# Performance work log

Measured on AMD Instinct MI355X. Metric: run time of the kernel, lower is better.

## Reference

```python
import jax, jax.numpy as jnp
from jax import lax
import numpy as np

INPUT = 80
H1 = 100
H2 = 50


def _lstm_layer(x, Wih, Whh, bih, bhh):
    """PyTorch-semantics single-layer LSTM, batch_first.
    x: [B,T,I]; Wih: [4H,I]; Whh: [4H,H]; biases: [4H]. Gate order: i,f,g,o.
    Returns full hidden sequence [B,T,H]."""
    B, T, _ = x.shape
    H = Whh.shape[1]
    # precompute input projections for all timesteps (one big GEMM)
    pre = jnp.einsum('bti,gi->tbg', x, Wih) + (bih + bhh)  # [T,B,4H]

    def step(carry, p):
        h, c = carry
        gates = p + h @ Whh.T  # [B,4H]
        i, f, g, o = jnp.split(gates, 4, axis=-1)
        i = jax.nn.sigmoid(i)
        f = jax.nn.sigmoid(f)
        g = jnp.tanh(g)
        o = jax.nn.sigmoid(o)
        c = f * c + i * g
        h = o * jnp.tanh(c)
        return (h, c), h

    h0 = jnp.zeros((B, H), x.dtype)
    (_, _), hs = lax.scan(step, (h0, h0), pre)  # hs: [T,B,H]
    return jnp.transpose(hs, (1, 0, 2))  # [B,T,H]


def setup_inputs() -> dict:
    key = jax.random.key(0)
    ks = jax.random.split(key, 9)
    B, T = 1024, 512
    s1 = 1.0 / np.sqrt(H1)
    s2 = 1.0 / np.sqrt(H2)
    return {
        'x': jax.random.normal(ks[0], (B, T, INPUT), dtype=jnp.float32),
        'Wih1': jax.random.uniform(ks[1], (4 * H1, INPUT), jnp.float32, -s1, s1),
        'Whh1': jax.random.uniform(ks[2], (4 * H1, H1), jnp.float32, -s1, s1),
        'bih1': jax.random.uniform(ks[3], (4 * H1,), jnp.float32, -s1, s1),
        'bhh1': jax.random.uniform(ks[4], (4 * H1,), jnp.float32, -s1, s1),
        'Wih2': jax.random.uniform(ks[5], (4 * H2, H1), jnp.float32, -s2, s2),
        'Whh2': jax.random.uniform(ks[6], (4 * H2, H2), jnp.float32, -s2, s2),
        'bih2': jax.random.uniform(ks[7], (4 * H2,), jnp.float32, -s2, s2),
        'bhh2': jax.random.uniform(ks[8], (4 * H2,), jnp.float32, -s2, s2),
    }


def reference(x, Wih1, Whh1, bih1, bhh1, Wih2, Whh2, bih2, bhh2):
    # Dropout layers are identity in eval mode.
    h1 = _lstm_layer(x, Wih1, Whh1, bih1, bhh1)   # [B,T,100]
    h2 = _lstm_layer(h1, Wih2, Whh2, bih2, bhh2)  # [B,T,50]
    return h2[:, -1, :]                            # [B,50]
```

## Files before the change

kernel.cpp:

```cpp
#include <hip/hip_runtime.h>

#define BT 1024
#define TT 512

__device__ __forceinline__ float sig_(float x) { return 1.f / (1.f + __expf(-x)); }
__device__ __forceinline__ float th_(float x)  { return 1.f - 2.f / (1.f + __expf(2.f * x)); }

#define PIN4(v) asm volatile("" : "+v"((v).x), "+v"((v).y), "+v"((v).z), "+v"((v).w))
#define PIN2(v) asm volatile("" : "+v"((v).x), "+v"((v).y))

template <int KS, int KPAD, int KH, int N, bool XMODE>
__device__ __forceinline__ void gp_stage(
    const float* __restrict__ A, const float* __restrict__ W,
    float (&As)[128][KPAD], float (&Bs)[KPAD][64],
    int tid, int n0, int by, int t0, int k0)
{
    constexpr int NQH = KH / 4;
#pragma unroll
    for (int ii = tid; ii < 128 * NQH; ii += 256) {
        int r = ii / NQH, q = ii % NQH;
        const float* src;
        if (XMODE) {
            int b  = (by & 7) * 128 + r;
            int tl = by >> 3;
            src = A + ((size_t)b * TT + (t0 + tl)) * KS;
        } else {
            src = A + (size_t)(by * 128 + r) * KS;
        }
        float4 v = *(const float4*)(src + k0 + q * 4);
        As[r][q * 4 + 0] = v.x; As[r][q * 4 + 1] = v.y;
        As[r][q * 4 + 2] = v.z; As[r][q * 4 + 3] = v.w;
    }
#pragma unroll
    for (int ii = tid; ii < 64 * NQH; ii += 256) {
        int n = ii & 63, kq = ii >> 6;
        float4 v = make_float4(0.f, 0.f, 0.f, 0.f);
        if (n0 + n < N) v = *(const float4*)(W + (size_t)(n0 + n) * KS + k0 + kq * 4);
        Bs[kq * 4 + 0][n] = v.x; Bs[kq * 4 + 1][n] = v.y;
        Bs[kq * 4 + 2][n] = v.z; Bs[kq * 4 + 3][n] = v.w;
    }
}

template <int KPAD, int KH>
__device__ __forceinline__ void gp_compute(
    const float (&As)[128][KPAD], const float (&Bs)[KPAD][64],
    float (&acc)[8][4], int tx, int ty)
{
    for (int kk = 0; kk < KH; kk += 4) {
        float4 bv0 = *(const float4*)&Bs[kk + 0][tx * 4];
        float4 bv1 = *(const float4*)&Bs[kk + 1][tx * 4];
        float4 bv2 = *(const float4*)&Bs[kk + 2][tx * 4];
        float4 bv3 = *(const float4*)&Bs[kk + 3][tx * 4];
#pragma unroll
        for (int i = 0; i < 8; i++) {
            float4 av = *(const float4*)&As[ty + 16 * i][kk];
            acc[i][0] = fmaf(av.x, bv0.x, acc[i][0]);
            acc[i][0] = fmaf(av.y, bv1.x, acc[i][0]);
            acc[i][0] = fmaf(av.z, bv2.x, acc[i][0]);
            acc[i][0] = fmaf(av.w, bv3.x, acc[i][0]);
            acc[i][1] = fmaf(av.x, bv0.y, acc[i][1]);
            acc[i][1] = fmaf(av.y, bv1.y, acc[i][1]);
            acc[i][1] = fmaf(av.z, bv2.y, acc[i][1]);
            acc[i][1] = fmaf(av.w, bv3.y, acc[i][1]);
            acc[i][2] = fmaf(av.x, bv0.z, acc[i][2]);
            acc[i][2] = fmaf(av.y, bv1.z, acc[i][2]);
            acc[i][2] = fmaf(av.z, bv2.z, acc[i][2]);
            acc[i][2] = fmaf(av.w, bv3.z, acc[i][2]);
            acc[i][3] = fmaf(av.x, bv0.w, acc[i][3]);
            acc[i][3] = fmaf(av.y, bv1.w, acc[i][3]);
            acc[i][3] = fmaf(av.z, bv2.w, acc[i][3]);
            acc[i][3] = fmaf(av.w, bv3.w, acc[i][3]);
        }
    }
}

template <int KS, int KPAD, int KH0, int N, bool XMODE>
__global__ __launch_bounds__(256, 4) void gemm_pre(
    const float* __restrict__ A, const float* __restrict__ W,
    const float* __restrict__ bih, const float* __restrict__ bhh,
    float* __restrict__ out, int t0)
{
    constexpr int KH1 = KS - KH0;
    __shared__ __align__(16) float As[128][KPAD];
    __shared__ __align__(16) float Bs[KPAD][64];
    const int tid = threadIdx.x;
    const int n0 = blockIdx.x * 64;
    const int by = blockIdx.y;
    const int Rbase = by * 128;
    const int tx = tid & 15, ty = tid >> 4;

    float acc[8][4];
#pragma unroll
    for (int i = 0; i < 8; i++)
#pragma unroll
        for (int j = 0; j < 4; j++) acc[i][j] = 0.f;

    gp_stage<KS, KPAD, KH0, N, XMODE>(A, W, As, Bs, tid, n0, by, t0, 0);
    __syncthreads();
    gp_compute<KPAD, KH0>(As, Bs, acc, tx, ty);
    __syncthreads();
    gp_stage<KS, KPAD, KH1, N, XMODE>(A, W, As, Bs, tid, n0, by, t0, KH0);
    __syncthreads();
    gp_compute<KPAD, KH1>(As, Bs, acc, tx, ty);

    int n = n0 + tx * 4;
    if (n < N) {
        float4 bias;
        bias.x = bih[n] + bhh[n];         bias.y = bih[n + 1] + bhh[n + 1];
        bias.z = bih[n + 2] + bhh[n + 2]; bias.w = bih[n + 3] + bhh[n + 3];
#pragma unroll
        for (int i = 0; i < 8; i++) {
            size_t R = (size_t)Rbase + ty + 16 * i;
            float4 o;
            o.x = acc[i][0] + bias.x; o.y = acc[i][1] + bias.y;
            o.z = acc[i][2] + bias.z; o.w = acc[i][3] + bias.w;
            *(float4*)(out + R * N + n) = o;
        }
    }
}

__global__ __launch_bounds__(512, 4) void rec1(
    const float* __restrict__ pre,
    const float* __restrict__ Whh,
    float* __restrict__ hseq,
    float* __restrict__ cst,
    int Tc, int first)
{
    __shared__ __align__(16) float hs[2][100];
    __shared__ __align__(16) float pres[2][800];
    __shared__ float gbuf[5 * 4 * 2 * 100];
    const int tid = threadIdx.x;
    const int b0 = blockIdx.x * 2;

    const bool comp = tid < 500;
    const int j  = tid % 100;
    const int kq = tid / 100;

    float4 w[4][5];
    if (comp) {
#pragma unroll
        for (int g = 0; g < 4; g++) {
            const float4* W4 = (const float4*)(Whh + (size_t)(g * 100 + j) * 100);
#pragma unroll
            for (int q = 0; q < 5; q++) w[g][q] = W4[kq * 5 + q];
        }
#pragma unroll
        for (int g = 0; g < 4; g++)
#pragma unroll
            for (int q = 0; q < 5; q++) PIN4(w[g][q]);
    }

    const bool upd = tid < 200;
    const int ub = tid / 100, uj = tid % 100;
    float c = 0.f;
    if (upd) {
        float h = 0.f;
        if (!first) {
            h = hseq[((size_t)(Tc - 1) * BT + b0 + ub) * 100 + uj];
            c = cst[(size_t)(b0 + ub) * 100 + uj];
        }
        hs[ub][uj] = h;
        ((float4*)pres[0])[tid] = ((const float4*)(pre + (size_t)b0 * 400))[tid];
    }
    __syncthreads();

    int cur = 0;
    for (int t = 0; t < Tc; t++) {
        int tn = (t + 1 < Tc) ? (t + 1) : t;
        float4 pf0;
        if (upd)
            pf0 = ((const float4*)(pre + (size_t)tn * BT * 400 + (size_t)b0 * 400))[tid];

        if (comp) {
            float acc[4][2];
#pragma unroll
            for (int g = 0; g < 4; g++) { acc[g][0] = 0.f; acc[g][1] = 0.f; }
            const float4* h0 = (const float4*)hs[0];
            const float4* h1 = (const float4*)hs[1];
#pragma unroll
            for (int q = 0; q < 5; q++) {
                int f = kq * 5 + q;
                float4 v0 = h0[f], v1 = h1[f];
#pragma unroll
                for (int g = 0; g < 4; g++) {
                    float4 wq = w[g][q];
                    acc[g][0] = fmaf(wq.x, v0.x, acc[g][0]);
                    acc[g][0] = fmaf(wq.y, v0.y, acc[g][0]);
                    acc[g][0] = fmaf(wq.z, v0.z, acc[g][0]);
                    acc[g][0] = fmaf(wq.w, v0.w, acc[g][0]);
                    acc[g][1] = fmaf(wq.x, v1.x, acc[g][1]);
                    acc[g][1] = fmaf(wq.y, v1.y, acc[g][1]);
                    acc[g][1] = fmaf(wq.z, v1.z, acc[g][1]);
                    acc[g][1] = fmaf(wq.w, v1.w, acc[g][1]);
                }
            }
#pragma unroll
            for (int g = 0; g < 4; g++) {
                gbuf[((kq * 4 + g) * 2 + 0) * 100 + j] = acc[g][0];
                gbuf[((kq * 4 + g) * 2 + 1) * 100 + j] = acc[g][1];
            }
        }
        __syncthreads();

        if (upd) {
            const float* pb = pres[cur];
            float s0 = 0.f, s1 = 0.f, s2 = 0.f, s3 = 0.f;
#pragma unroll
            for (int q = 0; q < 5; q++) {
                int base = q * 800;
                s0 += gbuf[base + (0 * 2 + ub) * 100 + uj];
                s1 += gbuf[base + (1 * 2 + ub) * 100 + uj];
                s2 += gbuf[base + (2 * 2 + ub) * 100 + uj];
                s3 += gbuf[base + (3 * 2 + ub) * 100 + uj];
            }
            float xi = s0 + pb[ub * 400 + uj];
            float xf = s1 + pb[ub * 400 + 100 + uj];
            float xg = s2 + pb[ub * 400 + 200 + uj];
            float xo = s3 + pb[ub * 400 + 300 + uj];
            float ii = sig_(xi), ff = sig_(xf), gg = th_(xg), oo = sig_(xo);
            c = ff * c + ii * gg;
            float h = oo * th_(c);
            hs[ub][uj] = h;
            hseq[((size_t)t * BT + b0 + ub) * 100 + uj] = h;
            ((float4*)pres[cur ^ 1])[tid] = pf0;
        }
        __syncthreads();
        cur ^= 1;
    }
    if (upd) cst[(size_t)(b0 + ub) * 100 + uj] = c;
}

__global__ __launch_bounds__(256, 4) void rec2(
    const float* __restrict__ pre2,
    const float* __restrict__ Whh,
    float* __restrict__ cst, float* __restrict__ hst,
    float* __restrict__ out,
    int Tc, int first)
{
    __shared__ __align__(16) float hs[2][50];
    __shared__ __align__(16) float pres[2][400];
    __shared__ float gbuf[5 * 4 * 2 * 50];
    const int tid = threadIdx.x;
    const int b0 = blockIdx.x * 2;

    const bool comp = tid < 250;
    const int j  = tid % 50;
    const int kq = tid / 50;

    float2 w[4][5];
    if (comp) {
#pragma unroll
        for (int g = 0; g < 4; g++) {
            const float2* W2 = (const float2*)(Whh + (size_t)(g * 50 + j) * 50);
#pragma unroll
            for (int q = 0; q < 5; q++) w[g][q] = W2[kq * 5 + q];
        }
#pragma unroll
        for (int g = 0; g < 4; g++)
#pragma unroll
            for (int q = 0; q < 5; q++) PIN2(w[g][q]);
    }

    const bool upd = tid < 100;
    const int ub = tid / 50, uj = tid % 50;
    float c = 0.f, hlast = 0.f;
    if (upd) {
        float h = 0.f;
        if (!first) {
            h = hst[(size_t)(b0 + ub) * 50 + uj];
            c = cst[(size_t)(b0 + ub) * 50 + uj];
        }
        hs[ub][uj] = h;
        hlast = h;
        ((float4*)pres[0])[tid] = ((const float4*)(pre2 + (size_t)b0 * 200))[tid];
    }
    __syncthreads();

    int cur = 0;
    for (int t = 0; t < Tc; t++) {
        int tn = (t + 1 < Tc) ? (t + 1) : t;
        float4 pf0;
        if (upd)
            pf0 = ((const float4*)(pre2 + (size_t)tn * BT * 200 + (size_t)b0 * 200))[tid];

        if (comp) {
            float acc[4][2];
#pragma unroll
            for (int g = 0; g < 4; g++) { acc[g][0] = 0.f; acc[g][1] = 0.f; }
            const float2* hA = (const float2*)hs[0];
            const float2* hB = (const float2*)hs[1];
#pragma unroll
            for (int q = 0; q < 5; q++) {
                int f = kq * 5 + q;
                float2 v0 = hA[f], v1 = hB[f];
#pragma unroll
                for (int g = 0; g < 4; g++) {
                    float2 wq = w[g][q];
                    acc[g][0] = fmaf(wq.x, v0.x, acc[g][0]);
                    acc[g][0] = fmaf(wq.y, v0.y, acc[g][0]);
                    acc[g][1] = fmaf(wq.x, v1.x, acc[g][1]);
                    acc[g][1] = fmaf(wq.y, v1.y, acc[g][1]);
                }
            }
#pragma unroll
            for (int g = 0; g < 4; g++) {
                gbuf[((kq * 4 + g) * 2 + 0) * 50 + j] = acc[g][0];
                gbuf[((kq * 4 + g) * 2 + 1) * 50 + j] = acc[g][1];
            }
        }
        __syncthreads();

        if (upd) {
            const float* pb = pres[cur];
            float s0 = 0.f, s1 = 0.f, s2 = 0.f, s3 = 0.f;
#pragma unroll
            for (int q = 0; q < 5; q++) {
                int base = q * 400;
                s0 += gbuf[base + (0 * 2 + ub) * 50 + uj];
                s1 += gbuf[base + (1 * 2 + ub) * 50 + uj];
                s2 += gbuf[base + (2 * 2 + ub) * 50 + uj];
                s3 += gbuf[base + (3 * 2 + ub) * 50 + uj];
            }
            float xi = s0 + pb[ub * 200 + uj];
            float xf = s1 + pb[ub * 200 + 50 + uj];
            float xg = s2 + pb[ub * 200 + 100 + uj];
            float xo = s3 + pb[ub * 200 + 150 + uj];
            float ii = sig_(xi), ff = sig_(xf), gg = th_(xg), oo = sig_(xo);
            c = ff * c + ii * gg;
            float h = oo * th_(c);
            hs[ub][uj] = h;
            hlast = h;
            ((float4*)pres[cur ^ 1])[tid] = pf0;
        }
        __syncthreads();
        cur ^= 1;
    }
    if (upd) {
        cst[(size_t)(b0 + ub) * 50 + uj] = c;
        hst[(size_t)(b0 + ub) * 50 + uj] = hlast;
        out[(size_t)(b0 + ub) * 50 + uj] = hlast;
    }
}

extern "C" void kernel_launch(void* const* d_in, const int* in_sizes, int n_in,
                              void* d_out, int out_size, void* d_ws, size_t ws_size,
                              hipStream_t stream)
{
    const float* x    = (const float*)d_in[0];
    const float* Wih1 = (const float*)d_in[1];
    const float* Whh1 = (const float*)d_in[2];
    const float* bih1 = (const float*)d_in[3];
    const float* bhh1 = (const float*)d_in[4];
    const float* Wih2 = (const float*)d_in[5];
    const float* Whh2 = (const float*)d_in[6];
    const float* bih2 = (const float*)d_in[7];
    const float* bhh2 = (const float*)d_in[8];
    float* out = (float*)d_out;
    float* ws  = (float*)d_ws;

    int Tc = 64;
    auto need = [](int tc) -> size_t {
        return ((size_t)tc * 1024 * (400 + 100 + 200) +
                (size_t)1024 * 100 + (size_t)1024 * 50 * 2) * sizeof(float);
    };
    while (Tc > 1 && need(Tc) > ws_size) Tc >>= 1;

    float* pre1 = ws;
    float* h1s  = pre1 + (size_t)Tc * 1024 * 400;
    float* pre2 = h1s  + (size_t)Tc * 1024 * 100;
    float* c1   = pre2 + (size_t)Tc * 1024 * 200;
    float* c2   = c1 + 1024 * 100;
    float* h2st = c2 + 1024 * 50;

    const int nch = TT / Tc;
    for (int ch = 0; ch < nch; ch++) {
        int t0 = ch * Tc;
        gemm_pre<80, 40, 40, 400, true ><<<dim3(7, Tc * 8), 256, 0, stream>>>(
            x, Wih1, bih1, bhh1, pre1, t0);
        rec1<<<dim3(512), dim3(512), 0, stream>>>(pre1, Whh1, h1s, c1, Tc, ch == 0 ? 1 : 0);
        gemm_pre<100, 52, 52, 200, false><<<dim3(4, Tc * 8), 256, 0, stream>>>(
            h1s, Wih2, bih2, bhh2, pre2, 0);
        rec2<<<dim3(512), dim3(256), 0, stream>>>(pre2, Whh2, c2, h2st, out, Tc, ch == 0 ? 1 : 0);
    }
}
```

Measured before the change: 2.693 ms.

## Widen GEMM N-tile to 128 and restructure rec1 to 4 batches per 1024-thread block

```diff
diff --git a/kernel.cpp b/kernel.cpp
--- a/kernel.cpp
+++ b/kernel.cpp
@@ -5,14 +5,11 @@
 
 __device__ __forceinline__ float sig_(float x) { return 1.f / (1.f + __expf(-x)); }
 __device__ __forceinline__ float th_(float x)  { return 1.f - 2.f / (1.f + __expf(2.f * x)); }
-
-#define PIN4(v) asm volatile("" : "+v"((v).x), "+v"((v).y), "+v"((v).z), "+v"((v).w))
-#define PIN2(v) asm volatile("" : "+v"((v).x), "+v"((v).y))
 
 template <int KS, int KPAD, int KH, int N, bool XMODE>
 __device__ __forceinline__ void gp_stage(
     const float* __restrict__ A, const float* __restrict__ W,
-    float (&As)[128][KPAD], float (&Bs)[KPAD][64],
+    float (&As)[128][KPAD], float (&Bs)[KPAD][128],
     int tid, int n0, int by, int t0, int k0)
 {
     constexpr int NQH = KH / 4;
@@ -27,13 +24,11 @@
         } else {
             src = A + (size_t)(by * 128 + r) * KS;
         }
-        float4 v = *(const float4*)(src + k0 + q * 4);
-        As[r][q * 4 + 0] = v.x; As[r][q * 4 + 1] = v.y;
-        As[r][q * 4 + 2] = v.z; As[r][q * 4 + 3] = v.w;
-    }
-#pragma unroll
-    for (int ii = tid; ii < 64 * NQH; ii += 256) {
-        int n = ii & 63, kq = ii >> 6;
+        *(float4*)&As[r][q * 4] = *(const float4*)(src + k0 + q * 4);
+    }
+#pragma unroll
+    for (int ii = tid; ii < 128 * NQH; ii += 256) {
+        int n = ii & 127, kq = ii >> 7;
         float4 v = make_float4(0.f, 0.f, 0.f, 0.f);
         if (n0 + n < N) v = *(const float4*)(W + (size_t)(n0 + n) * KS + k0 + kq * 4);
         Bs[kq * 4 + 0][n] = v.x; Bs[kq * 4 + 1][n] = v.y;
@@ -43,57 +38,62 @@
 
 template <int KPAD, int KH>
 __device__ __forceinline__ void gp_compute(
-    const float (&As)[128][KPAD], const float (&Bs)[KPAD][64],
-    float (&acc)[8][4], int tx, int ty)
+    const float (&As)[128][KPAD], const float (&Bs)[KPAD][128],
+    float (&acc)[8][8], int tx, int ty)
 {
     for (int kk = 0; kk < KH; kk += 4) {
-        float4 bv0 = *(const float4*)&Bs[kk + 0][tx * 4];
-        float4 bv1 = *(const float4*)&Bs[kk + 1][tx * 4];
-        float4 bv2 = *(const float4*)&Bs[kk + 2][tx * 4];
-        float4 bv3 = *(const float4*)&Bs[kk + 3][tx * 4];
+        float4 bv[4][2];
+#pragma unroll
+        for (int r = 0; r < 4; r++) {
+            bv[r][0] = *(const float4*)&Bs[kk + r][tx * 8];
+            bv[r][1] = *(const float4*)&Bs[kk + r][tx * 8 + 4];
+        }
 #pragma unroll
         for (int i = 0; i < 8; i++) {
             float4 av = *(const float4*)&As[ty + 16 * i][kk];
-            acc[i][0] = fmaf(av.x, bv0.x, acc[i][0]);
-            acc[i][0] = fmaf(av.y, bv1.x, acc[i][0]);
-            acc[i][0] = fmaf(av.z, bv2.x, acc[i][0]);
-            acc[i][0] = fmaf(av.w, bv3.x, acc[i][0]);
-            acc[i][1] = fmaf(av.x, bv0.y, acc[i][1]);
-            acc[i][1] = fmaf(av.y, bv1.y, acc[i][1]);
-            acc[i][1] = fmaf(av.z, bv2.y, acc[i][1]);
-            acc[i][1] = fmaf(av.w, bv3.y, acc[i][1]);
-            acc[i][2] = fmaf(av.x, bv0.z, acc[i][2]);
-            acc[i][2] = fmaf(av.y, bv1.z, acc[i][2]);
-            acc[i][2] = fmaf(av.z, bv2.z, acc[i][2]);
-            acc[i][2] = fmaf(av.w, bv3.z, acc[i][2]);
-            acc[i][3] = fmaf(av.x, bv0.w, acc[i][3]);
-            acc[i][3] = fmaf(av.y, bv1.w, acc[i][3]);
-            acc[i][3] = fmaf(av.z, bv2.w, acc[i][3]);
-            acc[i][3] = fmaf(av.w, bv3.w, acc[i][3]);
+#pragma unroll
+            for (int s = 0; s < 2; s++) {
+                acc[i][s*4+0] = fmaf(av.x, bv[0][s].x, acc[i][s*4+0]);
+                acc[i][s*4+0] = fmaf(av.y, bv[1][s].x, acc[i][s*4+0]);
+                acc[i][s*4+0] = fmaf(av.z, bv[2][s].x, acc[i][s*4+0]);
+                acc[i][s*4+0] = fmaf(av.w, bv[3][s].x, acc[i][s*4+0]);
+                acc[i][s*4+1] = fmaf(av.x, bv[0][s].y, acc[i][s*4+1]);
+                acc[i][s*4+1] = fmaf(av.y, bv[1][s].y, acc[i][s*4+1]);
+                acc[i][s*4+1] = fmaf(av.z, bv[2][s].y, acc[i][s*4+1]);
+                acc[i][s*4+1] = fmaf(av.w, bv[3][s].y, acc[i][s*4+1]);
+                acc[i][s*4+2] = fmaf(av.x, bv[0][s].z, acc[i][s*4+2]);
+                acc[i][s*4+2] = fmaf(av.y, bv[1][s].z, acc[i][s*4+2]);
+                acc[i][s*4+2] = fmaf(av.z, bv[2][s].z, acc[i][s*4+2]);
+                acc[i][s*4+2] = fmaf(av.w, bv[3][s].z, acc[i][s*4+2]);
+                acc[i][s*4+3] = fmaf(av.x, bv[0][s].w, acc[i][s*4+3]);
+                acc[i][s*4+3] = fmaf(av.y, bv[1][s].w, acc[i][s*4+3]);
+                acc[i][s*4+3] = fmaf(av.z, bv[2][s].w, acc[i][s*4+3]);
+                acc[i][s*4+3] = fmaf(av.w, bv[3][s].w, acc[i][s*4+3]);
+            }
         }
     }
 }
 
 template <int KS, int KPAD, int KH0, int N, bool XMODE>
-__global__ __launch_bounds__(256, 4) void gemm_pre(
+__global__ __launch_bounds__(256, 3) void gemm_pre(
     const float* __restrict__ A, const float* __restrict__ W,
     const float* __restrict__ bih, const float* __restrict__ bhh,
     float* __restrict__ out, int t0)
 {
     constexpr int KH1 = KS - KH0;
     __shared__ __align__(16) float As[128][KPAD];
-    __shared__ __align__(16) float Bs[KPAD][64];
+    __shared__ __align__(16) float Bs[KPAD][128];
     const int tid = threadIdx.x;
-    const int n0 = blockIdx.x * 64;
+    const int n0 = blockIdx.x * 128;
     const int by = blockIdx.y;
     const int Rbase = by * 128;
     const int tx = tid & 15, ty = tid >> 4;
 
-    float acc[8][4];
+    float acc[8][8];
 #pragma unroll
     for (int i = 0; i < 8; i++)
 #pragma unroll
-        for (int j = 0; j < 4; j++) acc[i][j] = 0.f;
+        for (int j = 0; j < 8; j++) acc[i][j] = 0.f;
 
     gp_stage<KS, KPAD, KH0, N, XMODE>(A, W, As, Bs, tid, n0, by, t0, 0);
     __syncthreads();
@@ -103,54 +103,53 @@
     __syncthreads();
     gp_compute<KPAD, KH1>(As, Bs, acc, tx, ty);
 
-    int n = n0 + tx * 4;
-    if (n < N) {
-        float4 bias;
-        bias.x = bih[n] + bhh[n];         bias.y = bih[n + 1] + bhh[n + 1];
-        bias.z = bih[n + 2] + bhh[n + 2]; bias.w = bih[n + 3] + bhh[n + 3];
-#pragma unroll
-        for (int i = 0; i < 8; i++) {
-            size_t R = (size_t)Rbase + ty + 16 * i;
-            float4 o;
-            o.x = acc[i][0] + bias.x; o.y = acc[i][1] + bias.y;
-            o.z = acc[i][2] + bias.z; o.w = acc[i][3] + bias.w;
-            *(float4*)(out + R * N + n) = o;
-        }
-    }
-}
-
-__global__ __launch_bounds__(512, 4) void rec1(
+#pragma unroll
+    for (int s = 0; s < 2; s++) {
+        int n = n0 + tx * 8 + s * 4;
+        if (n < N) {
+            float4 bias;
+            bias.x = bih[n] + bhh[n];         bias.y = bih[n + 1] + bhh[n + 1];
+            bias.z = bih[n + 2] + bhh[n + 2]; bias.w = bih[n + 3] + bhh[n + 3];
+#pragma unroll
+            for (int i = 0; i < 8; i++) {
+                size_t R = (size_t)Rbase + ty + 16 * i;
+                float4 o;
+                o.x = acc[i][s*4+0] + bias.x; o.y = acc[i][s*4+1] + bias.y;
+                o.z = acc[i][s*4+2] + bias.z; o.w = acc[i][s*4+3] + bias.w;
+                *(float4*)(out + R * N + n) = o;
+            }
+        }
+    }
+}
+
+__global__ __launch_bounds__(1024, 2) void rec1(
     const float* __restrict__ pre,
     const float* __restrict__ Whh,
     float* __restrict__ hseq,
     float* __restrict__ cst,
     int Tc, int first)
 {
-    __shared__ __align__(16) float hs[2][100];
-    __shared__ __align__(16) float pres[2][800];
-    __shared__ float gbuf[5 * 4 * 2 * 100];
+    __shared__ __align__(16) float hs[4][100];
+    __shared__ __align__(16) float pres[2][1600];
+    __shared__ float gbuf[10 * 4 * 4 * 104];
     const int tid = threadIdx.x;
-    const int b0 = blockIdx.x * 2;
-
-    const bool comp = tid < 500;
+    const int b0 = blockIdx.x * 4;
+
+    const bool comp = tid < 1000;
     const int j  = tid % 100;
     const int kq = tid / 100;
 
-    float4 w[4][5];
+    float2 w[4][5];
     if (comp) {
 #pragma unroll
         for (int g = 0; g < 4; g++) {
-            const float4* W4 = (const float4*)(Whh + (size_t)(g * 100 + j) * 100);
-#pragma unroll
-            for (int q = 0; q < 5; q++) w[g][q] = W4[kq * 5 + q];
-        }
-#pragma unroll
-        for (int g = 0; g < 4; g++)
-#pragma unroll
-            for (int q = 0; q < 5; q++) PIN4(w[g][q]);
-    }
-
-    const bool upd = tid < 200;
+            const float2* W2 = (const float2*)(Whh + (size_t)(g * 100 + j) * 100 + kq * 10);
+#pragma unroll
+            for (int q = 0; q < 5; q++) w[g][q] = W2[q];
+        }
+    }
+
+    const bool upd = tid < 400;
     const int ub = tid / 100, uj = tid % 100;
     float c = 0.f;
     if (upd) {
@@ -172,33 +171,46 @@
             pf0 = ((const float4*)(pre + (size_t)tn * BT * 400 + (size_t)b0 * 400))[tid];
 
         if (comp) {
-            float acc[4][2];
-#pragma unroll
-            for (int g = 0; g < 4; g++) { acc[g][0] = 0.f; acc[g][1] = 0.f; }
-            const float4* h0 = (const float4*)hs[0];
-            const float4* h1 = (const float4*)hs[1];
-#pragma unroll
-            for (int q = 0; q < 5; q++) {
+            float acc[4][4];
+            const float2* h0 = (const float2*)hs[0];
+            const float2* h1 = (const float2*)hs[1];
+            const float2* h2 = (const float2*)hs[2];
+            const float2* h3 = (const float2*)hs[3];
+            {
+                int f = kq * 5;
+                float2 v0 = h0[f], v1 = h1[f], v2 = h2[f], v3 = h3[f];
+#pragma unroll
+                for (int g = 0; g < 4; g++) {
+                    float2 wq = w[g][0];
+                    float a0 = wq.x * v0.x; a0 = fmaf(wq.y, v0.y, a0);
+                    float a1 = wq.x * v1.x; a1 = fmaf(wq.y, v1.y, a1);
+                    float a2 = wq.x * v2.x; a2 = fmaf(wq.y, v2.y, a2);
+                    float a3 = wq.x * v3.x; a3 = fmaf(wq.y, v3.y, a3);
+                    acc[g][0] = a0; acc[g][1] = a1; acc[g][2] = a2; acc[g][3] = a3;
+                }
+            }
+#pragma unroll
+            for (int q = 1; q < 5; q++) {
                 int f = kq * 5 + q;
-                float4 v0 = h0[f], v1 = h1[f];
+                float2 v0 = h0[f], v1 = h1[f], v2 = h2[f], v3 = h3[f];
 #pragma unroll
                 for (int g = 0; g < 4; g++) {
-                    float4 wq = w[g][q];
+                    float2 wq = w[g][q];
                     acc[g][0] = fmaf(wq.x, v0.x, acc[g][0]);
                     acc[g][0] = fmaf(wq.y, v0.y, acc[g][0]);
-                    acc[g][0] = fmaf(wq.z, v0.z, acc[g][0]);
-                    acc[g][0] = fmaf(wq.w, v0.w, acc[g][0]);
                     acc[g][1] = fmaf(wq.x, v1.x, acc[g][1]);
                     acc[g][1] = fmaf(wq.y, v1.y, acc[g][1]);
-                    acc[g][1] = fmaf(wq.z, v1.z, acc[g][1]);
-                    acc[g][1] = fmaf(wq.w, v1.w, acc[g][1]);
+                    acc[g][2] = fmaf(wq.x, v2.x, acc[g][2]);
+                    acc[g][2] = fmaf(wq.y, v2.y, acc[g][2]);
+                    acc[g][3] = fmaf(wq.x, v3.x, acc[g][3]);
+                    acc[g][3] = fmaf(wq.y, v3.y, acc[g][3]);
                 }
             }
 #pragma unroll
-            for (int g = 0; g < 4; g++) {
-                gbuf[((kq * 4 + g) * 2 + 0) * 100 + j] = acc[g][0];
-                gbuf[((kq * 4 + g) * 2 + 1) * 100 + j] = acc[g][1];
-            }
+            for (int g = 0; g < 4; g++)
+#pragma unroll
+                for (int b = 0; b < 4; b++)
+                    gbuf[((kq * 4 + g) * 4 + b) * 104 + j] = acc[g][b];
         }
         __syncthreads();
 
@@ -206,12 +218,12 @@
             const float* pb = pres[cur];
             float s0 = 0.f, s1 = 0.f, s2 = 0.f, s3 = 0.f;
 #pragma unroll
-            for (int q = 0; q < 5; q++) {
-                int base = q * 800;
-                s0 += gbuf[base + (0 * 2 + ub) * 100 + uj];
-                s1 += gbuf[base + (1 * 2 + ub) * 100 + uj];
-                s2 += gbuf[base + (2 * 2 + ub) * 100 + uj];
-                s3 += gbuf[base + (3 * 2 + ub) * 100 + uj];
+            for (int q = 0; q < 10; q++) {
+                int base = q * 4 * 4 * 104;
+                s0 += gbuf[base + (0 * 4 + ub) * 104 + uj];
+                s1 += gbuf[base + (1 * 4 + ub) * 104 + uj];
+                s2 += gbuf[base + (2 * 4 + ub) * 104 + uj];
+                s3 += gbuf[base + (3 * 4 + ub) * 104 + uj];
             }
             float xi = s0 + pb[ub * 400 + uj];
             float xf = s1 + pb[ub * 400 + 100 + uj];
@@ -255,10 +267,6 @@
 #pragma unroll
             for (int q = 0; q < 5; q++) w[g][q] = W2[kq * 5 + q];
         }
-#pragma unroll
-        for (int g = 0; g < 4; g++)
-#pragma unroll
-            for (int q = 0; q < 5; q++) PIN2(w[g][q]);
     }
 
     const bool upd = tid < 100;
@@ -375,10 +383,10 @@
     const int nch = TT / Tc;
     for (int ch = 0; ch < nch; ch++) {
         int t0 = ch * Tc;
-        gemm_pre<80, 40, 40, 400, true ><<<dim3(7, Tc * 8), 256, 0, stream>>>(
+        gemm_pre<80, 40, 40, 400, true ><<<dim3(4, Tc * 8), 256, 0, stream>>>(
             x, Wih1, bih1, bhh1, pre1, t0);
-        rec1<<<dim3(512), dim3(512), 0, stream>>>(pre1, Whh1, h1s, c1, Tc, ch == 0 ? 1 : 0);
-        gemm_pre<100, 52, 52, 200, false><<<dim3(4, Tc * 8), 256, 0, stream>>>(
+        rec1<<<dim3(256), dim3(1024), 0, stream>>>(pre1, Whh1, h1s, c1, Tc, ch == 0 ? 1 : 0);
+        gemm_pre<100, 52, 52, 200, false><<<dim3(2, Tc * 8), 256, 0, stream>>>(
             h1s, Wih2, bih2, bhh2, pre2, 0);
         rec2<<<dim3(512), dim3(256), 0, stream>>>(pre2, Whh2, c2, h2st, out, Tc, ch == 0 ? 1 : 0);
     }
```

Result: no change. 2.728 ms (+1.3%).
